# Performance work log

Hardware: AMD Instinct MI355X
Metric: run time of the kernel (lower is better)

Reference implementation:

```python
import jax, jax.numpy as jnp
import numpy as np

# module hyperparameters (match init_kwargs)
PATCH = 4          # patch_size
STRIDE = 2         # patch_stride
CH = 64            # embedding_dim (latent channels)
N_ATOMS = 512      # num_embeddings
SPARSITY = 5       # sparsity_level
COMMIT = 0.25      # commitment_cost
EPS = 1e-10        # epsilon
PATCH_DIM = CH * PATCH * PATCH


def _hann(n):
    # torch.hann_window(periodic=False)
    return 0.5 * (1.0 - jnp.cos(2.0 * jnp.pi * jnp.arange(n, dtype=jnp.float32) / (n - 1)))


def setup_inputs() -> dict:
    key = jax.random.key(0)
    k1, k2 = jax.random.split(key)
    x = jax.random.normal(k1, (8, CH, 128, 128), dtype=jnp.float32)
    D = jax.random.normal(k2, (PATCH_DIM, N_ATOMS), dtype=jnp.float32) * 0.02
    # normalize_dictionary_(): L2-normalize atoms (columns)
    D = D / jnp.maximum(jnp.linalg.norm(D, axis=0, keepdims=True), EPS)
    return {"x": x, "dictionary": D}


def reference(x, dictionary):
    B, C, H, W = x.shape
    Ho = (H - PATCH) // STRIDE + 1
    Wo = (W - PATCH) // STRIDE + 1
    N = B * Ho * Wo

    # ---- unfold (im2col) : [B,C,Ho,Wo,P,P] ----
    row = (jnp.arange(Ho) * STRIDE)[:, None] + jnp.arange(PATCH)  # [Ho,P]
    col = (jnp.arange(Wo) * STRIDE)[:, None] + jnp.arange(PATCH)  # [Wo,P]
    ridx = row[:, None, :, None]   # [Ho,1,P,1]
    cidx = col[None, :, None, :]   # [1,Wo,1,P]
    patches = x[:, :, ridx, cidx]  # [B,C,Ho,Wo,P,P]
    # columns ordered (C, ph, pw) like torch F.unfold
    X = patches.transpose(0, 2, 3, 1, 4, 5).reshape(N, PATCH_DIM)  # [N, patch_dim]

    # ---- batch_topk_with_support sparse coding ----
    corr = X @ dictionary                 # [N, K]  (D^T X)^T
    gram = dictionary.T @ dictionary      # [K, K]
    support = jax.lax.top_k(jnp.abs(corr), SPARSITY)[1]           # [N, k]
    rhs = jnp.take_along_axis(corr, support, axis=1)              # [N, k]
    gram_sup = gram[support[:, :, None], support[:, None, :]]     # [N, k, k]
    gram_sup = gram_sup + EPS * jnp.eye(SPARSITY, dtype=x.dtype)
    values = jnp.linalg.solve(gram_sup, rhs[..., None])[..., 0]   # [N, k]

    # ---- reconstruct patch signals: X_hat = D[:,support] @ values ----
    codes = jnp.zeros((N, N_ATOMS), dtype=x.dtype).at[
        jnp.arange(N)[:, None], support].add(values)              # sparse -> dense codes
    X_hat = codes @ dictionary.T                                  # [N, patch_dim]

    # ---- Hann-window overlap-add fold ----
    w1 = _hann(PATCH)
    w2 = w1[:, None] * w1[None, :]                                # [P,P]
    patches_hat = X_hat.reshape(B, Ho, Wo, C, PATCH, PATCH).transpose(0, 3, 1, 2, 4, 5)
    num = jnp.zeros_like(x).at[:, :, ridx, cidx].add(patches_hat * w2)
    den = jnp.zeros((H, W), dtype=x.dtype).at[ridx, cidx].add(
        jnp.broadcast_to(w2, (Ho, Wo, PATCH, PATCH)))
    z_q = num / jnp.maximum(den, EPS)

    # ---- losses + straight-through ----
    e_latent = jnp.mean((jax.lax.stop_gradient(z_q) - x) ** 2)
    dl_latent = jnp.mean((z_q - jax.lax.stop_gradient(x)) ** 2)
    loss = dl_latent + COMMIT * e_latent
    quantized = x + jax.lax.stop_gradient(z_q - x)
    return quantized, loss
```

## Files before the change

### kernel.cpp

```cpp
#include <hip/hip_runtime.h>

#define CHN    64
#define NATOMS 512
#define PDIM   1024
#define KSP    5
#define HO_    63
#define WO_    63
#define NPATCH 31752
#define MPAD   31872
#define HH     128
#define WW     128
#define MT     16
#define OUT_N  8388608
#define DELTA  6e-3f
#define QGUARD 2.5e-3f
#define FBLK   2048
#define RPB    ((NPATCH + 15) / 16)

typedef _Float16 f16;
typedef _Float16 f16x8 __attribute__((ext_vector_type(8)));
typedef float    f32x4 __attribute__((ext_vector_type(4)));
typedef float    f32x2 __attribute__((ext_vector_type(2)));

static __device__ __forceinline__ void gload_lds16(const void* g, void* l) {
    __builtin_amdgcn_global_load_lds(
        (const __attribute__((address_space(1))) unsigned int*)g,
        (__attribute__((address_space(3))) unsigned int*)l, 16, 0, 0);
}

static __device__ inline f32x2 fma2(f32x2 a, f32x2 b, f32x2 c) {
#if __has_builtin(__builtin_elementwise_fma)
    return __builtin_elementwise_fma(a, b, c);
#else
    f32x2 r; r.x = fmaf(a.x, b.x, c.x); r.y = fmaf(a.y, b.y, c.y); return r;
#endif
}

static __device__ __forceinline__ unsigned mk_key32(float v, int idx) {
    unsigned vb = __float_as_uint(v);
    unsigned ab = vb & 0x7FFFFFFFu;
    return ((ab >> 11) << 11) | ((unsigned)(1023 - idx) << 1) | (vb >> 31);
}
static __device__ __forceinline__ int key32_idx(unsigned k) {
    return 1023 - (int)((k >> 1) & 1023u);
}

#define CEU(s, i, j) { unsigned _a = s[i], _b = s[j]; \
                       s[i] = _a > _b ? _a : _b; s[j] = _a > _b ? _b : _a; }

#define SORT8(s) \
    CEU(s,0,1) CEU(s,2,3) CEU(s,4,5) CEU(s,6,7) \
    CEU(s,0,2) CEU(s,1,3) CEU(s,4,6) CEU(s,5,7) \
    CEU(s,1,2) CEU(s,5,6) \
    CEU(s,0,4) CEU(s,1,5) CEU(s,2,6) CEU(s,3,7) \
    CEU(s,2,4) CEU(s,3,5) \
    CEU(s,1,2) CEU(s,3,4) CEU(s,5,6)

#define MERGE8(s, a, b) { \
    unsigned L[8]; \
    L[0] = a[0] > b[7] ? a[0] : b[7]; L[1] = a[1] > b[6] ? a[1] : b[6]; \
    L[2] = a[2] > b[5] ? a[2] : b[5]; L[3] = a[3] > b[4] ? a[3] : b[4]; \
    L[4] = a[4] > b[3] ? a[4] : b[3]; L[5] = a[5] > b[2] ? a[5] : b[2]; \
    L[6] = a[6] > b[1] ? a[6] : b[1]; L[7] = a[7] > b[0] ? a[7] : b[0]; \
    CEU(L,0,4) CEU(L,1,5) CEU(L,2,6) CEU(L,3,7) \
    CEU(L,0,2) CEU(L,1,3) CEU(L,4,6) CEU(L,5,7) \
    CEU(L,0,1) CEU(L,2,3) CEU(L,4,5) CEU(L,6,7) \
    for (int _i = 0; _i < 8; ++_i) s[_i] = L[_i]; }

__global__ __launch_bounds__(256) void gram_kernel(const float* __restrict__ D,
                                                   float* __restrict__ gram) {
    __shared__ float Ti[64][32];
    __shared__ float Tj[64][32];
    const int tid = threadIdx.x;
    const int i0 = blockIdx.x * 32, j0 = blockIdx.y * 32;
    const int ri  = tid >> 3;
    const int rj0 = (tid & 7) * 4;
    float acc[4] = {0.f, 0.f, 0.f, 0.f};
    for (int k0 = 0; k0 < PDIM; k0 += 64) {
        __syncthreads();
#pragma unroll
        for (int s = 0; s < 8; ++s) {
            int e = tid + 256 * s;
            int kk = e >> 5, col = e & 31;
            Ti[kk][col] = D[(size_t)(k0 + kk) * NATOMS + i0 + col];
            Tj[kk][col] = D[(size_t)(k0 + kk) * NATOMS + j0 + col];
        }
        __syncthreads();
#pragma unroll 4
        for (int kk = 0; kk < 64; ++kk) {
            float ti = Ti[kk][ri];
#pragma unroll
            for (int q = 0; q < 4; ++q)
                acc[q] = fmaf(ti, Tj[kk][rj0 + q], acc[q]);
        }
    }
#pragma unroll
    for (int q = 0; q < 4; ++q)
        gram[(size_t)(i0 + ri) * NATOMS + j0 + rj0 + q] = acc[q];
}

__global__ __launch_bounds__(256) void extract_kernel(const float* __restrict__ x,
                                                      f16* __restrict__ Xh) {
    __shared__ float xs[16][4][129];
    const int bid = blockIdx.x;
    const int cg  = bid & 3;
    const int t   = bid >> 2;
    const int ho  = t % HO_;
    const int b   = t / HO_;

    for (int i = threadIdx.x; i < 64 * 32; i += 256) {
        int r = i >> 5;
        int q = i & 31;
        int c = r >> 2, pr = r & 3;
        float4 v = *(const float4*)(x + ((size_t)(b * CHN + cg * 16 + c) * HH
                                         + (2 * ho + pr)) * WW + q * 4);
        xs[c][pr][q * 4 + 0] = v.x;
        xs[c][pr][q * 4 + 1] = v.y;
        xs[c][pr][q * 4 + 2] = v.z;
        xs[c][pr][q * 4 + 3] = v.w;
    }
    __syncthreads();

    for (int p = threadIdx.x; p < WO_ * 16; p += 256) {
        int wo = p >> 4;
        int c  = p & 15;
        f16 h[16];
#pragma unroll
        for (int pr = 0; pr < 4; ++pr)
#pragma unroll
            for (int pc = 0; pc < 4; ++pc)
                h[pr * 4 + pc] = (f16)xs[c][pr][2 * wo + pc];
        int n = (b * HO_ + ho) * WO_ + wo;
        f16x8 v0, v1;
#pragma unroll
        for (int i2 = 0; i2 < 8; ++i2) { v0[i2] = h[i2]; v1[i2] = h[8 + i2]; }
        f16* dh = Xh + (size_t)n * PDIM + (cg * 16 + c) * 16;
        *(f16x8*)dh = v0; *(f16x8*)(dh + 8) = v1;
    }
}

__global__ __launch_bounds__(256) void dtrans_kernel(const float* __restrict__ D,
                                                     f16* __restrict__ Dth,
                                                     f16* __restrict__ Dtl) {
    __shared__ float ts[64][65];
    const int k0 = blockIdx.x * 64;
    const int n0 = blockIdx.y * 64;

    for (int i = threadIdx.x; i < 64 * 16; i += 256) {
        int r = i >> 4;
        int q = i & 15;
        float4 v = *(const float4*)(D + (size_t)(k0 + r) * NATOMS + n0 + q * 4);
        ts[r][q * 4 + 0] = v.x;
        ts[r][q * 4 + 1] = v.y;
        ts[r][q * 4 + 2] = v.z;
        ts[r][q * 4 + 3] = v.w;
    }
    __syncthreads();

    {
        int i = threadIdx.x;
        int nn = i >> 2, q = i & 3;
        f16 h[16], l[16];
#pragma unroll
        for (int j = 0; j < 16; ++j) {
            float v = ts[q * 16 + j][nn];
            f16 hh = (f16)v;
            h[j] = hh;
            l[j] = (f16)(v - (float)hh);
        }
        f16x8 h0, h1, l0, l1;
#pragma unroll
        for (int j = 0; j < 8; ++j) { h0[j] = h[j]; h1[j] = h[8 + j]; l0[j] = l[j]; l1[j] = l[8 + j]; }
        f16* dh = Dth + (size_t)(n0 + nn) * PDIM + k0 + q * 16;
        f16* dl = Dtl + (size_t)(n0 + nn) * PDIM + k0 + q * 16;
        *(f16x8*)dh = h0; *(f16x8*)(dh + 8) = h1;
        *(f16x8*)dl = l0; *(f16x8*)(dl + 8) = l1;
    }
}

__global__ __launch_bounds__(512) void gemm_kernel(const f16* __restrict__ Xh,
                                                   const f16* __restrict__ Dth,
                                                   f16* __restrict__ corr) {
    __shared__ char lds[98304];
    const int tid  = threadIdx.x;
    const int lane = tid & 63;
    const int wave = tid >> 6;
    const size_t arow0 = (size_t)blockIdx.x * 128;
    const int    brow0 = blockIdx.y * 256;
    const int wm = wave >> 2;
    const int wn = wave & 3;

    f32x4 acc[4][4];
#pragma unroll
    for (int m = 0; m < 4; ++m)
#pragma unroll
        for (int n = 0; n < 4; ++n) acc[m][n] = (f32x4){0.f, 0.f, 0.f, 0.f};

    const char* asrc[2]; int adst[2];
#pragma unroll
    for (int i = 0; i < 2; ++i) {
        int p = tid * 16 + i * 8192;
        int row = p >> 7, sc = ((p >> 4) & 7) ^ (row & 7);
        asrc[i] = (const char*)Xh + (arow0 + row) * 2048 + sc * 16;
        adst[i] = p;
    }
    const char* bsrc[4]; int bdst[4];
#pragma unroll
    for (int i = 0; i < 4; ++i) {
        int p = tid * 16 + i * 8192;
        int row = p >> 7, sc = ((p >> 4) & 7) ^ (row & 7);
        bsrc[i] = (const char*)Dth + (size_t)(brow0 + row) * 2048 + sc * 16;
        bdst[i] = 16384 + p;
    }

    int aoff[4][2], boff[4][2];
#pragma unroll
    for (int m = 0; m < 4; ++m)
#pragma unroll
        for (int ks = 0; ks < 2; ++ks) {
            int row = wm * 64 + m * 16 + (lane & 15);
            int ch  = (ks * 4 + (lane >> 4)) ^ (row & 7);
            aoff[m][ks] = row * 128 + ch * 16;
        }
#pragma unroll
    for (int n = 0; n < 4; ++n)
#pragma unroll
        for (int ks = 0; ks < 2; ++ks) {
            int row = wn * 64 + n * 16 + (lane & 15);
            int ch  = (ks * 4 + (lane >> 4)) ^ (row & 7);
            boff[n][ks] = 16384 + row * 128 + ch * 16;
        }

#pragma unroll
    for (int i = 0; i < 2; ++i) gload_lds16(asrc[i], lds + adst[i]);
#pragma unroll
    for (int i = 0; i < 4; ++i) gload_lds16(bsrc[i], lds + bdst[i]);
#pragma unroll
    for (int i = 0; i < 2; ++i) asrc[i] += 128;
#pragma unroll
    for (int i = 0; i < 4; ++i) bsrc[i] += 128;
    __syncthreads();

    int bufo = 0;
    for (int kt = 0; kt < 16; ++kt) {
        const int nbuf = bufo ^ 49152;
        if (kt + 1 < 16) {
#pragma unroll
            for (int i = 0; i < 2; ++i) { gload_lds16(asrc[i], lds + nbuf + adst[i]); asrc[i] += 128; }
#pragma unroll
            for (int i = 0; i < 4; ++i) { gload_lds16(bsrc[i], lds + nbuf + bdst[i]); bsrc[i] += 128; }
        }
#pragma unroll
        for (int ks = 0; ks < 2; ++ks) {
            f16x8 a[4], b[4];
#pragma unroll
            for (int m = 0; m < 4; ++m) a[m] = *(const f16x8*)(lds + bufo + aoff[m][ks]);
#pragma unroll
            for (int n = 0; n < 4; ++n) b[n] = *(const f16x8*)(lds + bufo + boff[n][ks]);
#pragma unroll
            for (int m = 0; m < 4; ++m)
#pragma unroll
                for (int n = 0; n < 4; ++n)
                    acc[m][n] = __builtin_amdgcn_mfma_f32_16x16x32_f16(a[m], b[n], acc[m][n], 0, 0, 0);
        }
        if (kt + 1 < 16) { __syncthreads(); bufo = nbuf; }
    }

#pragma unroll
    for (int m = 0; m < 4; ++m) {
        size_t row_b = arow0 + wm * 64 + m * 16 + (lane >> 4) * 4;
#pragma unroll
        for (int n = 0; n < 4; ++n) {
            int col = brow0 + wn * 64 + n * 16 + (lane & 15);
#pragma unroll
            for (int i = 0; i < 4; ++i)
                corr[(row_b + i) * NATOMS + col] = (f16)acc[m][n][i];
        }
    }
}

__global__ __launch_bounds__(512) void topred_kernel(const f16* __restrict__ corr,
                                                     unsigned* __restrict__ topk) {
    const int tid = threadIdx.x;
    const int sl  = tid & 31;
    const int hw  = tid >> 5;
    const int np  = blockIdx.x * 16 + hw;

    const f16* row = corr + (size_t)np * NATOMS;
    const f16* cr = row + sl * 16;
    f16x8 c0 = *(const f16x8*)cr;
    f16x8 c1 = *(const f16x8*)(cr + 8);
    unsigned k[16];
#pragma unroll
    for (int j = 0; j < 8; ++j) {
        k[j]     = mk_key32((float)c0[j], sl * 16 + j);
        k[8 + j] = mk_key32((float)c1[j], sl * 16 + 8 + j);
    }

    unsigned a[8], b8[8];
#pragma unroll
    for (int i = 0; i < 8; ++i) { a[i] = k[i]; b8[i] = k[8 + i]; }
    SORT8(a)
    SORT8(b8)
    unsigned s[8];
    MERGE8(s, a, b8)
#pragma unroll
    for (int off = 16; off; off >>= 1) {
        unsigned p[8];
#pragma unroll
        for (int i = 0; i < 8; ++i) p[i] = (unsigned)__shfl_xor((int)s[i], off);
        MERGE8(s, s, p)
    }

    if (sl == 0 && np < NPATCH) {
        float v0 = (float)row[key32_idx(s[0])], v1 = (float)row[key32_idx(s[1])];
        float v2 = (float)row[key32_idx(s[2])], v3 = (float)row[key32_idx(s[3])];
        float v4 = (float)row[key32_idx(s[4])], v5 = (float)row[key32_idx(s[5])];
        float v6 = (float)row[key32_idx(s[6])], v7 = (float)row[key32_idx(s[7])];
        uint4* dst = (uint4*)(topk + (size_t)np * 16);
        dst[0] = make_uint4(s[0], s[1], s[2], s[3]);
        dst[1] = make_uint4(s[4], s[5], s[6], s[7]);
        dst[2] = make_uint4(__float_as_uint(v0), __float_as_uint(v1),
                            __float_as_uint(v2), __float_as_uint(v3));
        dst[3] = make_uint4(__float_as_uint(v4), __float_as_uint(v5),
                            __float_as_uint(v6), __float_as_uint(v7));
    }
}

__global__ __launch_bounds__(64) void topfin_kernel(const unsigned* __restrict__ topk,
                                                    const f16* __restrict__ corr,
                                                    const float* __restrict__ x,
                                                    const float* __restrict__ D,
                                                    const float* __restrict__ gram,
                                                    int* __restrict__ sup_out,
                                                    float* __restrict__ val_out) {
    const int lane = threadIdx.x & 63;
    const int half = lane >> 5;
    const int sl   = lane & 31;
    const int hw   = threadIdx.x >> 5;
    const int np   = blockIdx.x * 2 + hw;

    unsigned s[8];
    float    tval[8];
    {
        const uint4* src = (const uint4*)(topk + (size_t)np * 16);
        uint4 s0 = src[0], s1 = src[1], v0 = src[2], v1 = src[3];
        s[0] = s0.x; s[1] = s0.y; s[2] = s0.z; s[3] = s0.w;
        s[4] = s1.x; s[5] = s1.y; s[6] = s1.z; s[7] = s1.w;
        tval[0] = __uint_as_float(v0.x); tval[1] = __uint_as_float(v0.y);
        tval[2] = __uint_as_float(v0.z); tval[3] = __uint_as_float(v0.w);
        tval[4] = __uint_as_float(v1.x); tval[5] = __uint_as_float(v1.y);
        tval[6] = __uint_as_float(v1.z); tval[7] = __uint_as_float(v1.w);
    }
    int tidx[8];
#pragma unroll
    for (int r = 0; r < 8; ++r) tidx[r] = key32_idx(s[r]);

    const float a5 = fabsf(tval[KSP - 1]);
    const float lo = fmaxf(a5 - DELTA, 0.0f);
    const float hi = a5 + DELTA;
    const unsigned lokey = (__float_as_uint(fmaxf(lo - QGUARD, 0.0f)) >> 11) << 11;

    int   nfinal = 0, fidx[KSP];
    float fval[KSP];
    int   nwin = 0, widx[8];
    float wvf[8];
#pragma unroll
    for (int r = 0; r < KSP; ++r) {
        if (fabsf(tval[r]) > hi) { fidx[nfinal] = tidx[r]; fval[nfinal] = tval[r]; ++nfinal; }
        else                     { widx[nwin] = tidx[r]; wvf[nwin] = tval[r]; ++nwin; }
    }
#pragma unroll
    for (int r = KSP; r < 8; ++r) {
        if (fabsf(tval[r]) >= lo && nwin < 8) { widx[nwin] = tidx[r]; wvf[nwin] = tval[r]; ++nwin; }
    }

    if (s[7] >= lokey) {
        const f16* cr = corr + (size_t)np * NATOMS + sl * 16;
        f16x8 c0 = *(const f16x8*)cr;
        f16x8 c1 = *(const f16x8*)(cr + 8);
        unsigned k[16];
        float vbuf[16];
#pragma unroll
        for (int j = 0; j < 8; ++j) {
            vbuf[j]     = (float)c0[j];
            vbuf[8 + j] = (float)c1[j];
            k[j]        = mk_key32(vbuf[j], sl * 16 + j);
            k[8 + j]    = mk_key32(vbuf[8 + j], sl * 16 + 8 + j);
        }
#pragma unroll
        for (int i = 0; i < 16; ++i) {
            bool ex = (k[i] < s[7]) && (k[i] >= lokey);
            unsigned m = (unsigned)(__ballot(ex) >> (half * 32));
            while (m && nwin < 8) {
                int l = __ffs(m) - 1; m &= m - 1;
                unsigned kk = (unsigned)__shfl((int)k[i], l + half * 32);
                float vv2 = __shfl(vbuf[i], l + half * 32);
                if (fabsf(vv2) >= lo) { widx[nwin] = key32_idx(kk); wvf[nwin] = vv2; ++nwin; }
            }
        }
    }

    const int need = KSP - nfinal;
    if (nwin == need) {
        for (int w = 0; w < nwin; ++w) { fidx[nfinal] = widx[w]; fval[nfinal] = wvf[w]; ++nfinal; }
    } else {
        int bb_ = np / (HO_ * WO_);
        int rr  = np - bb_ * (HO_ * WO_);
        int ho2 = rr / WO_;
        int wo2 = rr - ho2 * WO_;
        const float* xb = x + (size_t)bb_ * CHN * HH * WW;
        double wv64[8];
        for (int w = 0; w < nwin; ++w) {
            int at = widx[w];
            double sd = 0.0;
#pragma unroll
            for (int t = 0; t < 32; ++t) {
                int kk = sl + (t << 5);
                int c  = kk >> 4, pr = (kk >> 2) & 3, pc = kk & 3;
                float xv = xb[((size_t)c * HH + (2 * ho2 + pr)) * WW + 2 * wo2 + pc];
                float dv = D[(size_t)kk * NATOMS + at];
                sd = fma((double)xv, (double)dv, sd);
            }
            for (int off = 16; off; off >>= 1) sd += __shfl_xor(sd, off);
            wv64[w] = sd;
        }
        unsigned taken = 0u;
        for (int scnt = 0; scnt < need; ++scnt) {
            int best = -1; double bbv = -1.0;
            for (int w = 0; w < nwin; ++w) {
                if ((taken >> w) & 1u) continue;
                double aw = fabs(wv64[w]);
                if (aw > bbv || (aw == bbv && best >= 0 && widx[w] < widx[best])) { bbv = aw; best = w; }
            }
            taken |= 1u << best;
            fidx[nfinal] = widx[best];
            fval[nfinal] = (float)wv64[best];
            ++nfinal;
        }
    }

    float A[KSP][KSP], bb[KSP];
    {
        float gv = 0.f;
        if (sl < 25) {
            int gi = sl / 5, gj = sl - 5 * gi;
            gv = gram[(size_t)fidx[gi] * NATOMS + fidx[gj]];
        }
#pragma unroll
        for (int i = 0; i < KSP; ++i)
#pragma unroll
            for (int j = 0; j < KSP; ++j)
                A[i][j] = __shfl(gv, i * 5 + j + half * 32);
    }
#pragma unroll
    for (int i = 0; i < KSP; ++i) bb[i] = fval[i];
#pragma unroll
    for (int c = 0; c < KSP; ++c) {
        float inv = 1.0f / A[c][c];
#pragma unroll
        for (int r = 0; r < KSP; ++r) {
            if (r > c) {
                float f = A[r][c] * inv;
#pragma unroll
                for (int cc = 0; cc < KSP; ++cc)
                    if (cc > c) A[r][cc] -= f * A[c][cc];
                bb[r] -= f * bb[c];
            }
        }
    }
#pragma unroll
    for (int r = KSP - 1; r >= 0; --r) {
        float t = bb[r];
#pragma unroll
        for (int cc = 0; cc < KSP; ++cc)
            if (cc > r) t -= A[r][cc] * bb[cc];
        bb[r] = t / A[r][r];
    }
    if (sl == 0) {
#pragma unroll
        for (int i = 0; i < KSP; ++i) {
            sup_out[(size_t)np * KSP + i] = fidx[i];
            val_out[(size_t)np * KSP + i] = bb[i];
        }
    }
}

__global__ __launch_bounds__(256) void reconp_kernel(const float* __restrict__ x,
                                                     const f16* __restrict__ Dth,
                                                     const f16* __restrict__ Dtl,
                                                     const int* __restrict__ sup,
                                                     const float* __restrict__ val,
                                                     float* __restrict__ out,
                                                     double* __restrict__ rpart) {
    __shared__ f32x4 zbuf[16][65];
    __shared__ double red[4];
    const int lane = threadIdx.x & 63;
    const int wave = threadIdx.x >> 6;
    const int n0   = blockIdx.x * 16;

#pragma unroll
    for (int it = 0; it < 4; ++it) {
        const int nl = it * 4 + wave;
        const int n  = n0 + nl;
        if (n < NPATCH) {
            const int*   sp = sup + (size_t)n * KSP;
            const float* vp = val + (size_t)n * KSP;
            float z[16];
#pragma unroll
            for (int i = 0; i < 16; ++i) z[i] = 0.f;
#pragma unroll
            for (int t = 0; t < KSP; ++t) {
                int a = sp[t]; float v = vp[t];
                const f16* dh = Dth + (size_t)a * PDIM + lane * 16;
                const f16* dl = Dtl + (size_t)a * PDIM + lane * 16;
                f16x8 h0 = *(const f16x8*)dh, h1 = *(const f16x8*)(dh + 8);
                f16x8 l0 = *(const f16x8*)dl, l1 = *(const f16x8*)(dl + 8);
#pragma unroll
                for (int i = 0; i < 8; ++i) {
                    z[i]     = fmaf(v, (float)h0[i] + (float)l0[i], z[i]);
                    z[8 + i] = fmaf(v, (float)h1[i] + (float)l1[i], z[8 + i]);
                }
            }
            zbuf[nl][lane] = (f32x4){ z[5], z[6], z[9], z[10] };
        }
    }
    __syncthreads();

    double sq = 0.0;
#pragma unroll
    for (int k = 0; k < 4; ++k) {
        int f  = threadIdx.x + 256 * k;
        int c  = f >> 4;
        int nl = f & 15;
        int n  = n0 + nl;
        if (n < NPATCH) {
            int b  = n / (HO_ * WO_);
            int r  = n - b * (HO_ * WO_);
            int ho = r / WO_, wo = r - ho * WO_;
            f32x4 zv = zbuf[nl][c];
            size_t base = ((size_t)(b * CHN + c) * HH + (2 * ho + 1)) * WW + (2 * wo + 1);
            float x0 = x[base],      x1 = x[base + 1];
            float x2 = x[base + WW], x3 = x[base + WW + 1];
            out[base]          = x0 + (zv.x - x0);
            out[base + 1]      = x1 + (zv.y - x1);
            out[base + WW]     = x2 + (zv.z - x2);
            out[base + WW + 1] = x3 + (zv.w - x3);
            float d0 = zv.x - x0, d1 = zv.y - x1, d2 = zv.z - x2, d3 = zv.w - x3;
            sq += (double)d0 * d0 + (double)d1 * d1 + (double)d2 * d2 + (double)d3 * d3;
        }
    }

    for (int off = 32; off; off >>= 1) sq += __shfl_xor(sq, off);
    if (lane == 0) red[wave] = sq;
    __syncthreads();
    if (threadIdx.x == 0) rpart[blockIdx.x] = red[0] + red[1] + red[2] + red[3];
}

__global__ __launch_bounds__(256) void border_kernel(const float* __restrict__ x,
                                                     float* __restrict__ out,
                                                     double* __restrict__ bpart) {
    const int plane = blockIdx.x;
    const float* xp = x + (size_t)plane * HH * WW;
    float* op = out + (size_t)plane * HH * WW;
    double sq = 0.0;
    for (int idx = threadIdx.x; idx < 508; idx += 256) {
        int i, j;
        if (idx < 128)      { i = 0;         j = idx;       }
        else if (idx < 256) { i = 127;       j = idx - 128; }
        else if (idx < 382) { i = idx - 255; j = 0;         }
        else                { i = idx - 381; j = 127;       }
        float xv = xp[i * WW + j];
        op[i * WW + j] = xv + (0.0f - xv);
        sq += (double)xv * xv;
    }
    for (int off = 32; off; off >>= 1) sq += __shfl_xor(sq, off);
    __shared__ double red[4];
    const int lane = threadIdx.x & 63, wv = threadIdx.x >> 6;
    if (lane == 0) red[wv] = sq;
    __syncthreads();
    if (threadIdx.x == 0) bpart[blockIdx.x] = red[0] + red[1] + red[2] + red[3];
}

__global__ __launch_bounds__(256) void loss2_kernel(const double* __restrict__ rpart,
                                                    const double* __restrict__ bpart,
                                                    float* __restrict__ out) {
    double s = 0.0;
    for (int i = threadIdx.x; i < RPB; i += 256) s += rpart[i];
    for (int i = threadIdx.x; i < 512; i += 256) s += bpart[i];
    for (int off = 32; off; off >>= 1) s += __shfl_xor(s, off);
    __shared__ double red[4];
    const int lane = threadIdx.x & 63, wv = threadIdx.x >> 6;
    if (lane == 0) red[wv] = s;
    __syncthreads();
    if (threadIdx.x == 0) {
        double m = (red[0] + red[1] + red[2] + red[3]) / (double)OUT_N;
        out[OUT_N] = (float)(m + 0.25 * m);
    }
}

__global__ __launch_bounds__(256) void corr_kernel_fb(const float* __restrict__ x,
                                                      const float* __restrict__ D,
                                                      const float* __restrict__ gram,
                                                      int* __restrict__ sup_out,
                                                      float* __restrict__ val_out) {
    __shared__ float pt[256 * MT];
    __shared__ float corrbuf[MT][NATOMS];
    __shared__ int   sup_s[MT][KSP];
    __shared__ float rhs_s[MT][KSP];

    const int tid  = threadIdx.x;
    const int lane = tid & 63;
    const int wave = tid >> 6;
    const int n0   = blockIdx.x * MT;
    const int sp  = lane & 15;
    const int spr = lane >> 4;

    int n = n0 + sp;
    bool pvalid = (n < NPATCH);
    int b = 0, ho = 0, wo = 0;
    if (pvalid) {
        b = n / (HO_ * WO_);
        int r = n - b * (HO_ * WO_);
        ho = r / WO_;
        wo = r - ho * WO_;
    }

    f32x2 accP[2][8];
#pragma unroll
    for (int a = 0; a < 2; ++a)
#pragma unroll
        for (int g = 0; g < 8; ++g) accP[a][g] = (f32x2)(0.f);

    for (int chunk = 0; chunk < 4; ++chunk) {
        __syncthreads();
#pragma unroll
        for (int t = 0; t < 4; ++t) {
            int s = wave + 4 * t;
            int c = chunk * 16 + s;
            float2 va = make_float2(0.f, 0.f), vb = make_float2(0.f, 0.f);
            if (pvalid) {
                const float* px = x + (((size_t)b * CHN + c) * HH + (2 * ho + spr)) * WW + 2 * wo;
                va = *(const float2*)px;
                vb = *(const float2*)(px + 2);
            }
            int kl = (s * 16 + spr * 4) * MT + sp;
            pt[kl]          = va.x;
            pt[kl + MT]     = va.y;
            pt[kl + 2 * MT] = vb.x;
            pt[kl + 3 * MT] = vb.y;
        }
        __syncthreads();
        const float* Dp = D + (size_t)chunk * 256 * NATOMS + 2 * tid;
#pragma unroll 4
        for (int k = 0; k < 256; ++k) {
            float2 dv = *(const float2*)(Dp + (size_t)k * NATOMS);
            f32x2 d00 = {dv.x, dv.x}, d11 = {dv.y, dv.y};
#pragma unroll
            for (int q = 0; q < 4; ++q) {
                const float4 f = *(const float4*)&pt[k * MT + 4 * q];
                f32x2 flo = {f.x, f.y}, fhi = {f.z, f.w};
                accP[0][2 * q]     = fma2(flo, d00, accP[0][2 * q]);
                accP[1][2 * q]     = fma2(flo, d11, accP[1][2 * q]);
                accP[0][2 * q + 1] = fma2(fhi, d00, accP[0][2 * q + 1]);
                accP[1][2 * q + 1] = fma2(fhi, d11, accP[1][2 * q + 1]);
            }
        }
    }
#pragma unroll
    for (int g = 0; g < 8; ++g) {
        *(float2*)&corrbuf[2 * g][2 * tid]     = make_float2(accP[0][g].x, accP[1][g].x);
        *(float2*)&corrbuf[2 * g + 1][2 * tid] = make_float2(accP[0][g].y, accP[1][g].y);
    }
    __syncthreads();

    for (int pi = 0; pi < 4; ++pi) {
        int p  = wave * 4 + pi;
        int np = n0 + p;
        if (np >= NPATCH) continue;
        float v[8], av[8];
#pragma unroll
        for (int i = 0; i < 8; ++i) {
            v[i]  = corrbuf[p][lane + 64 * i];
            av[i] = fabsf(v[i]);
        }
        unsigned usedm = 0u;
        int   top_i[KSP];
        float top_v[KSP];
#pragma unroll
        for (int r = 0; r < KSP; ++r) {
            float ba = -1.0f, bv = 0.0f;
            int   bi = 0x7FFFFFFF;
#pragma unroll
            for (int i = 0; i < 8; ++i) {
                if (!((usedm >> i) & 1u)) {
                    int idx = lane + 64 * i;
                    if (av[i] > ba || (av[i] == ba && idx < bi)) { ba = av[i]; bi = idx; bv = v[i]; }
                }
            }
            for (int off = 32; off; off >>= 1) {
                float oa = __shfl_xor(ba, off);
                int   oi = __shfl_xor(bi, off);
                float ov = __shfl_xor(bv, off);
                if (oa > ba || (oa == ba && oi < bi)) { ba = oa; bi = oi; bv = ov; }
            }
            top_i[r] = bi; top_v[r] = bv;
            if (lane == (bi & 63)) usedm |= (1u << (bi >> 6));
        }
        const float a5 = fabsf(top_v[KSP - 1]);
        const float lo = a5 - DELTA, hi = a5 + DELTA;
        int   nfinal = 0, fidx[KSP];
        float fval[KSP];
        int   nwin = 0, widx[8];
        float wvf[8];
#pragma unroll
        for (int r = 0; r < KSP; ++r) {
            if (fabsf(top_v[r]) > hi) { fidx[nfinal] = top_i[r]; fval[nfinal] = top_v[r]; ++nfinal; }
            else if (nwin < 8)        { widx[nwin] = top_i[r]; wvf[nwin] = top_v[r]; ++nwin; }
        }
#pragma unroll
        for (int i = 0; i < 8; ++i) {
            bool ex = (((usedm >> i) & 1u) == 0u) && (av[i] >= lo);
            unsigned long long m = __ballot(ex);
            while (m && nwin < 8) {
                int l = __ffsll(m) - 1; m &= m - 1;
                widx[nwin] = l + 64 * i;
                wvf[nwin]  = __shfl(v[i], l);
                ++nwin;
            }
        }
        const int need = KSP - nfinal;
        if (nwin == need) {
            for (int w = 0; w < nwin; ++w) { fidx[nfinal] = widx[w]; fval[nfinal] = wvf[w]; ++nfinal; }
        } else {
            int bb_ = np / (HO_ * WO_);
            int rr  = np - bb_ * (HO_ * WO_);
            int ho2 = rr / WO_;
            int wo2 = rr - ho2 * WO_;
            const float* xb = x + (size_t)bb_ * CHN * HH * WW;
            double wv64[8];
            for (int w = 0; w < nwin; ++w) {
                int a = widx[w];
                double s = 0.0;
                for (int t = 0; t < 16; ++t) {
                    int k  = lane + (t << 6);
                    int c  = k >> 4, pr = (k >> 2) & 3, pc = k & 3;
                    float xv = xb[((size_t)c * HH + (2 * ho2 + pr)) * WW + 2 * wo2 + pc];
                    float dv = D[(size_t)k * NATOMS + a];
                    s = fma((double)xv, (double)dv, s);
                }
                for (int off = 32; off; off >>= 1) s += __shfl_xor(s, off);
                wv64[w] = s;
            }
            unsigned taken = 0u;
            for (int scnt = 0; scnt < need; ++scnt) {
                int best = -1; double bbv = -1.0;
                for (int w = 0; w < nwin; ++w) {
                    if ((taken >> w) & 1u) continue;
                    double aw = fabs(wv64[w]);
                    if (aw > bbv || (aw == bbv && best >= 0 && widx[w] < widx[best])) { bbv = aw; best = w; }
                }
                taken |= 1u << best;
                fidx[nfinal] = widx[best];
                fval[nfinal] = (float)wv64[best];
                ++nfinal;
            }
        }
        if (lane == 0) {
#pragma unroll
            for (int r = 0; r < KSP; ++r) { sup_s[p][r] = fidx[r]; rhs_s[p][r] = fval[r]; }
        }
    }
    __syncthreads();

    if (tid < MT) {
        int p = tid, np = n0 + p;
        if (np < NPATCH) {
            int s[KSP];
            double A[KSP][KSP], bb[KSP];
#pragma unroll
            for (int i = 0; i < KSP; ++i) { s[i] = sup_s[p][i]; bb[i] = (double)rhs_s[p][i]; }
#pragma unroll
            for (int i = 0; i < KSP; ++i)
#pragma unroll
                for (int j = 0; j < KSP; ++j)
                    A[i][j] = (double)gram[(size_t)s[i] * NATOMS + s[j]] + (i == j ? 1e-10 : 0.0);
#pragma unroll
            for (int c = 0; c < KSP; ++c) {
                double inv = 1.0 / A[c][c];
#pragma unroll
                for (int r = 0; r < KSP; ++r) {
                    if (r > c) {
                        double f = A[r][c] * inv;
#pragma unroll
                        for (int cc = 0; cc < KSP; ++cc)
                            if (cc > c) A[r][cc] -= f * A[c][cc];
                        bb[r] -= f * bb[c];
                    }
                }
            }
#pragma unroll
            for (int r = KSP - 1; r >= 0; --r) {
                double t = bb[r];
#pragma unroll
                for (int cc = 0; cc < KSP; ++cc)
                    if (cc > r) t -= A[r][cc] * bb[cc];
                bb[r] = t / A[r][r];
            }
#pragma unroll
            for (int i = 0; i < KSP; ++i) {
                sup_out[(size_t)np * KSP + i] = s[i];
                val_out[(size_t)np * KSP + i] = (float)bb[i];
            }
        }
    }
}

__global__ __launch_bounds__(256) void recon_kernel_fb(const float* __restrict__ x,
                                                       const float* __restrict__ D,
                                                       const int* __restrict__ sup,
                                                       const float* __restrict__ val,
                                                       float* __restrict__ out,
                                                       double* __restrict__ partials) {
    double sqacc = 0.0;
    for (size_t o = (size_t)blockIdx.x * 256 + threadIdx.x; o < OUT_N; o += (size_t)FBLK * 256) {
        const int j = (int)(o & 127);
        const int i = (int)((o >> 7) & 127);
        const int c = (int)((o >> 14) & 63);
        const int b = (int)(o >> 20);
        const float xv = x[o];
        float z = 0.0f;
        const int pr = (i & 1) ? 1 : 2;
        const int pc = (j & 1) ? 1 : 2;
        const int ho = (i - pr) >> 1;
        const int wo = (j - pc) >> 1;
        if (ho >= 0 && ho < HO_ && wo >= 0 && wo < WO_) {
            const int n = (b * HO_ + ho) * WO_ + wo;
            const int k = c * 16 + pr * 4 + pc;
            const int*   sp5 = sup + (size_t)n * KSP;
            const float* vp5 = val + (size_t)n * KSP;
            float s = 0.0f;
#pragma unroll
            for (int t = 0; t < KSP; ++t)
                s = fmaf(vp5[t], D[(size_t)k * NATOMS + sp5[t]], s);
            z = s;
        }
        out[o] = xv + (z - xv);
        const float d = z - xv;
        sqacc += (double)d * (double)d;
    }
    for (int off = 32; off; off >>= 1) sqacc += __shfl_xor(sqacc, off);
    __shared__ double red[4];
    const int lane = threadIdx.x & 63, wv = threadIdx.x >> 6;
    if (lane == 0) red[wv] = sqacc;
    __syncthreads();
    if (threadIdx.x == 0) partials[blockIdx.x] = red[0] + red[1] + red[2] + red[3];
}

__global__ __launch_bounds__(256) void loss_kernel(const double* __restrict__ partials,
                                                   float* __restrict__ out) {
    double s = 0.0;
    for (int i = threadIdx.x; i < FBLK; i += 256) s += partials[i];
    for (int off = 32; off; off >>= 1) s += __shfl_xor(s, off);
    __shared__ double red[4];
    const int lane = threadIdx.x & 63, wv = threadIdx.x >> 6;
    if (lane == 0) red[wv] = s;
    __syncthreads();
    if (threadIdx.x == 0) {
        double m = (red[0] + red[1] + red[2] + red[3]) / (double)OUT_N;
        out[OUT_N] = (float)(m + 0.25 * m);
    }
}

extern "C" void kernel_launch(void* const* d_in, const int* in_sizes, int n_in,
                              void* d_out, int out_size, void* d_ws, size_t ws_size,
                              hipStream_t stream) {
    const float* x = (const float*)d_in[0];
    const float* D = (const float*)d_in[1];
    float* out = (float*)d_out;
    char* ws = (char*)d_ws;

    size_t off = 0;
    auto take = [&](size_t bytes) { char* p = ws + off; off += (bytes + 255) & ~(size_t)255; return p; };
    float*    gram     = (float*)take((size_t)NATOMS * NATOMS * 4);
    int*      sup      = (int*)take((size_t)NPATCH * KSP * 4);
    float*    val      = (float*)take((size_t)NPATCH * KSP * 4);
    double*   partials = (double*)take((size_t)FBLK * 8);
    double*   rpart    = (double*)take((size_t)RPB * 8);
    double*   bpart    = (double*)take((size_t)512 * 8);
    unsigned* topk     = (unsigned*)take((size_t)NPATCH * 16 * 4);
    f16*   Dth  = (f16*)take((size_t)NATOMS * PDIM * 2);
    f16*   Dtl  = (f16*)take((size_t)NATOMS * PDIM * 2);
    f16*   Xh   = (f16*)take((size_t)MPAD * PDIM * 2);
    f16*   corr = (f16*)take((size_t)MPAD * NATOMS * 2);
    const bool big = (off <= ws_size);

    if (big) {
        hipMemsetAsync(Xh + (size_t)NPATCH * PDIM, 0,
                       (size_t)(MPAD - NPATCH) * PDIM * sizeof(f16), stream);
        extract_kernel<<<8 * HO_ * 4, 256, 0, stream>>>(x, Xh);
        dtrans_kernel<<<dim3(16, 8), 256, 0, stream>>>(D, Dth, Dtl);
        gram_kernel<<<dim3(16, 16), 256, 0, stream>>>(D, gram);
        border_kernel<<<512, 256, 0, stream>>>(x, out, bpart);
        gemm_kernel<<<dim3(MPAD / 128, NATOMS / 256), 512, 0, stream>>>(Xh, Dth, corr);
        topred_kernel<<<(NPATCH + 15) / 16, 512, 0, stream>>>(corr, topk);
        topfin_kernel<<<NPATCH / 2, 64, 0, stream>>>(topk, corr, x, D, gram, sup, val);
        reconp_kernel<<<RPB, 256, 0, stream>>>(x, Dth, Dtl, sup, val, out, rpart);
        loss2_kernel<<<1, 256, 0, stream>>>(rpart, bpart, out);
    } else {
        gram_kernel<<<dim3(16, 16), 256, 0, stream>>>(D, gram);
        corr_kernel_fb<<<(NPATCH + MT - 1) / MT, 256, 0, stream>>>(x, D, gram, sup, val);
        recon_kernel_fb<<<FBLK, 256, 0, stream>>>(x, D, sup, val, out, partials);
        loss_kernel<<<1, 256, 0, stream>>>(partials, out);
    }
}
```

Measured before the change: 226.8 us.

## Restructure reconstruction to write full image rows with float4 stores

The reconstruction kernel now assigns one block per (batch, output row) of patches and stages the central 2x2 values of all 63 patches in shared memory as per-row planes. Each thread then writes contiguous float4 runs of two full image rows, which also fills the left and right border columns with zeros. The border kernel therefore only handles the top and bottom rows, using float4 accesses with one wave per plane. The aim is coalesced, vectorized global reads and writes in place of the scattered 2x2 scalar accesses. The cost is a larger shared-memory footprint per block and fewer, larger blocks.

```diff
diff --git a/kernel.cpp b/kernel.cpp
--- a/kernel.cpp
+++ b/kernel.cpp
@@ -15,7 +15,7 @@
 #define DELTA  6e-3f
 #define QGUARD 2.5e-3f
 #define FBLK   2048
-#define RPB    ((NPATCH + 15) / 16)
+#define RPB    (8 * HO_)
 
 typedef _Float16 f16;
 typedef _Float16 f16x8 __attribute__((ext_vector_type(8)));
@@ -493,17 +493,19 @@
                                                      const float* __restrict__ val,
                                                      float* __restrict__ out,
                                                      double* __restrict__ rpart) {
-    __shared__ f32x4 zbuf[16][65];
+    __shared__ float zplane[4][WO_][65];
     __shared__ double red[4];
     const int lane = threadIdx.x & 63;
     const int wave = threadIdx.x >> 6;
-    const int n0   = blockIdx.x * 16;
-
-#pragma unroll
-    for (int it = 0; it < 4; ++it) {
-        const int nl = it * 4 + wave;
-        const int n  = n0 + nl;
-        if (n < NPATCH) {
+    const int ho = blockIdx.x % HO_;
+    const int b  = blockIdx.x / HO_;
+    const int nbase = (b * HO_ + ho) * WO_;
+
+#pragma unroll
+    for (int it = 0; it < 16; ++it) {
+        const int wo = it * 4 + wave;
+        if (wo < WO_) {
+            const int n = nbase + wo;
             const int*   sp = sup + (size_t)n * KSP;
             const float* vp = val + (size_t)n * KSP;
             float z[16];
@@ -522,33 +524,37 @@
                     z[8 + i] = fmaf(v, (float)h1[i] + (float)l1[i], z[8 + i]);
                 }
             }
-            zbuf[nl][lane] = (f32x4){ z[5], z[6], z[9], z[10] };
+            zplane[0][wo][lane] = z[5];
+            zplane[1][wo][lane] = z[6];
+            zplane[2][wo][lane] = z[9];
+            zplane[3][wo][lane] = z[10];
         }
     }
     __syncthreads();
 
     double sq = 0.0;
 #pragma unroll
-    for (int k = 0; k < 4; ++k) {
-        int f  = threadIdx.x + 256 * k;
-        int c  = f >> 4;
-        int nl = f & 15;
-        int n  = n0 + nl;
-        if (n < NPATCH) {
-            int b  = n / (HO_ * WO_);
-            int r  = n - b * (HO_ * WO_);
-            int ho = r / WO_, wo = r - ho * WO_;
-            f32x4 zv = zbuf[nl][c];
-            size_t base = ((size_t)(b * CHN + c) * HH + (2 * ho + 1)) * WW + (2 * wo + 1);
-            float x0 = x[base],      x1 = x[base + 1];
-            float x2 = x[base + WW], x3 = x[base + WW + 1];
-            out[base]          = x0 + (zv.x - x0);
-            out[base + 1]      = x1 + (zv.y - x1);
-            out[base + WW]     = x2 + (zv.z - x2);
-            out[base + WW + 1] = x3 + (zv.w - x3);
-            float d0 = zv.x - x0, d1 = zv.y - x1, d2 = zv.z - x2, d3 = zv.w - x3;
-            sq += (double)d0 * d0 + (double)d1 * d1 + (double)d2 * d2 + (double)d3 * d3;
-        }
+    for (int k = 0; k < 16; ++k) {
+        int f = threadIdx.x + 256 * k;
+        int q = f & 31;
+        int c = (f >> 5) & 63;
+        int r = f >> 11;
+        const int prof = r * 2;
+        float4 zv;
+        zv.x = (q == 0)  ? 0.f : zplane[prof + 1][2 * q - 1][c];
+        zv.y = zplane[prof][2 * q][c];
+        zv.z = zplane[prof + 1][2 * q][c];
+        zv.w = (q == 31) ? 0.f : zplane[prof][2 * q + 1][c];
+        size_t base = ((size_t)(b * CHN + c) * HH + (2 * ho + 1 + r)) * WW + 4 * q;
+        float4 xv = *(const float4*)(x + base);
+        float4 ov;
+        ov.x = xv.x + (zv.x - xv.x);
+        ov.y = xv.y + (zv.y - xv.y);
+        ov.z = xv.z + (zv.z - xv.z);
+        ov.w = xv.w + (zv.w - xv.w);
+        *(float4*)(out + base) = ov;
+        float d0 = zv.x - xv.x, d1 = zv.y - xv.y, d2 = zv.z - xv.z, d3 = zv.w - xv.w;
+        sq += (double)d0 * d0 + (double)d1 * d1 + (double)d2 * d2 + (double)d3 * d3;
     }
 
     for (int off = 32; off; off >>= 1) sq += __shfl_xor(sq, off);
@@ -557,29 +563,25 @@
     if (threadIdx.x == 0) rpart[blockIdx.x] = red[0] + red[1] + red[2] + red[3];
 }
 
-__global__ __launch_bounds__(256) void border_kernel(const float* __restrict__ x,
-                                                     float* __restrict__ out,
-                                                     double* __restrict__ bpart) {
+__global__ __launch_bounds__(64) void border_kernel(const float* __restrict__ x,
+                                                    float* __restrict__ out,
+                                                    double* __restrict__ bpart) {
     const int plane = blockIdx.x;
-    const float* xp = x + (size_t)plane * HH * WW;
-    float* op = out + (size_t)plane * HH * WW;
-    double sq = 0.0;
-    for (int idx = threadIdx.x; idx < 508; idx += 256) {
-        int i, j;
-        if (idx < 128)      { i = 0;         j = idx;       }
-        else if (idx < 256) { i = 127;       j = idx - 128; }
-        else if (idx < 382) { i = idx - 255; j = 0;         }
-        else                { i = idx - 381; j = 127;       }
-        float xv = xp[i * WW + j];
-        op[i * WW + j] = xv + (0.0f - xv);
-        sq += (double)xv * xv;
-    }
+    const int t = threadIdx.x;
+    const int r = (t >> 5) ? 127 : 0;
+    const int q = t & 31;
+    size_t base = (size_t)plane * HH * WW + (size_t)r * WW + 4 * q;
+    float4 xv = *(const float4*)(x + base);
+    float4 ov;
+    ov.x = xv.x + (0.0f - xv.x);
+    ov.y = xv.y + (0.0f - xv.y);
+    ov.z = xv.z + (0.0f - xv.z);
+    ov.w = xv.w + (0.0f - xv.w);
+    *(float4*)(out + base) = ov;
+    double sq = (double)xv.x * xv.x + (double)xv.y * xv.y
+              + (double)xv.z * xv.z + (double)xv.w * xv.w;
     for (int off = 32; off; off >>= 1) sq += __shfl_xor(sq, off);
-    __shared__ double red[4];
-    const int lane = threadIdx.x & 63, wv = threadIdx.x >> 6;
-    if (lane == 0) red[wv] = sq;
-    __syncthreads();
-    if (threadIdx.x == 0) bpart[blockIdx.x] = red[0] + red[1] + red[2] + red[3];
+    if (threadIdx.x == 0) bpart[blockIdx.x] = sq;
 }
 
 __global__ __launch_bounds__(256) void loss2_kernel(const double* __restrict__ rpart,
@@ -901,7 +903,7 @@
         extract_kernel<<<8 * HO_ * 4, 256, 0, stream>>>(x, Xh);
         dtrans_kernel<<<dim3(16, 8), 256, 0, stream>>>(D, Dth, Dtl);
         gram_kernel<<<dim3(16, 16), 256, 0, stream>>>(D, gram);
-        border_kernel<<<512, 256, 0, stream>>>(x, out, bpart);
+        border_kernel<<<512, 64, 0, stream>>>(x, out, bpart);
         gemm_kernel<<<dim3(MPAD / 128, NATOMS / 256), 512, 0, stream>>>(Xh, Dth, corr);
         topred_kernel<<<(NPATCH + 15) / 16, 512, 0, stream>>>(corr, topk);
         topfin_kernel<<<NPATCH / 2, 64, 0, stream>>>(topk, corr, x, D, gram, sup, val);
```

Measured after the change: 251.3 us. 10.8% more time.
